# Performance work log

Measured on AMD Instinct MI355X. Metric: run time of the kernel, lower is better.

Reference implementation:

```python
import jax, jax.numpy as jnp
import numpy as np

NUM_HEADS = 16
ROPE_BASE = 2048.0


def _rope_tables(seq_len, head_dim, dtype):
    inv_freq = 1.0 / (ROPE_BASE ** (jnp.arange(0, head_dim, 2, dtype=jnp.float32) / head_dim))
    t = jnp.arange(seq_len, dtype=jnp.float32)
    freqs = jnp.einsum('i,j->ij', t, inv_freq)          # [N, D/2]
    emb = jnp.concatenate([freqs, freqs], axis=-1)       # [N, D]
    return jnp.cos(emb).astype(dtype), jnp.sin(emb).astype(dtype)


def _rotate_half(x):
    x1, x2 = jnp.split(x, 2, axis=-1)
    return jnp.concatenate([-x2, x1], axis=-1)


def setup_inputs() -> dict:
    key = jax.random.key(0)
    k1, k2, k3, k4 = jax.random.split(key, 4)
    B, N, C = 2, 2048, 1024
    x = jax.random.normal(k1, (B, N, C), dtype=jnp.float32)
    w_qkv = jax.random.normal(k2, (3 * C, C), dtype=jnp.float32) * (C ** -0.5)
    w_proj = jax.random.normal(k3, (C, C), dtype=jnp.float32) * (C ** -0.5)
    b_proj = jnp.zeros((C,), dtype=jnp.float32)
    key_padding_mask = jax.random.randint(k4, (B, N), 0, 2, dtype=jnp.int32)
    return {"x": x, "w_qkv": w_qkv, "w_proj": w_proj, "b_proj": b_proj,
            "key_padding_mask": key_padding_mask}


def reference(x, w_qkv, w_proj, b_proj, key_padding_mask):
    B, N, C = x.shape
    H = NUM_HEADS
    D = C // H
    scale = D ** -0.5

    qkv = x @ w_qkv.T                                    # [B, N, 3C]
    q, k, v = jnp.split(qkv, 3, axis=-1)
    # [B, N, C] -> [B, H, N, D]
    q = q.reshape(B, N, H, D).transpose(0, 2, 1, 3)
    k = k.reshape(B, N, H, D).transpose(0, 2, 1, 3)
    v = v.reshape(B, N, H, D).transpose(0, 2, 1, 3)

    cos, sin = _rope_tables(N, D, x.dtype)               # [N, D]
    q = q * cos + _rotate_half(q) * sin
    k = k * cos + _rotate_half(k) * sin

    attn = jnp.einsum('bhqd,bhkd->bhqk', q, k) * scale   # [B, H, N, N]
    mask = (key_padding_mask == 0)[:, None, None, :]     # [B, 1, 1, N]
    attn = jnp.where(mask, jnp.asarray(-1e9, attn.dtype), attn)
    attn = jax.nn.softmax(attn, axis=-1)

    out = jnp.einsum('bhqk,bhkd->bhqd', attn, v)         # [B, H, N, D]
    out = out.transpose(0, 2, 1, 3).reshape(B, N, C)
    return out @ w_proj.T + b_proj
```

## Files before the change

### kernel.cpp

```cpp
#include <hip/hip_runtime.h>


typedef __attribute__((ext_vector_type(8))) short          s16x8;
typedef __attribute__((ext_vector_type(8))) unsigned short u16x8;
typedef __attribute__((ext_vector_type(4))) unsigned short u16x4;
typedef __attribute__((ext_vector_type(4))) float          f32x4;

#define MFMA_BF16(a, b, c) __builtin_amdgcn_mfma_f32_16x16x32_bf16((a), (b), (c), 0, 0, 0)

#define GLD_TO_LDS(gp, lp) __builtin_amdgcn_global_load_lds(                  \
    (const __attribute__((address_space(1))) void*)(gp),                      \
    (__attribute__((address_space(3))) void*)(lp), 16, 0, 0)

__device__ __forceinline__ unsigned short f2bf(float f) {
    union { float f; unsigned int u; } v; v.f = f;
    unsigned int u = v.u;
    unsigned int r = u + 0x7FFFu + ((u >> 16) & 1u);
    return (unsigned short)(r >> 16);
}
__device__ __forceinline__ float bf2f(unsigned short h) {
    union { unsigned int u; float f; } v; v.u = ((unsigned int)h) << 16;
    return v.f;
}

__global__ __launch_bounds__(256) void prep(const float* __restrict__ x,
                                            const float* __restrict__ wqkv,
                                            const float* __restrict__ wproj,
                                            const int* __restrict__ m,
                                            unsigned short* __restrict__ xb,
                                            unsigned short* __restrict__ wqkvb,
                                            unsigned short* __restrict__ wprojb,
                                            float* __restrict__ fb) {
    int blk = blockIdx.x, tid = threadIdx.x;
    if (blk < 8192) {
        const float* src; unsigned short* dst; int i;
        if (blk < 4096)      { src = x;     dst = xb;     i = blk * 256 + tid; }
        else if (blk < 7168) { src = wqkv;  dst = wqkvb;  i = (blk - 4096) * 256 + tid; }
        else                 { src = wproj; dst = wprojb; i = (blk - 7168) * 256 + tid; }
        f32x4 v = ((const f32x4*)src)[i];
        u16x4 o;
        o[0] = f2bf(v[0]); o[1] = f2bf(v[1]); o[2] = f2bf(v[2]); o[3] = f2bf(v[3]);
        ((u16x4*)dst)[i] = o;
    } else {
        int i = (blk - 8192) * 256 + tid;
        fb[i] = (m[i] == 0) ? -1e5f : 0.0f;
    }
}

__global__ __launch_bounds__(256) void gemm_bt(const unsigned short* __restrict__ A,
                                               const unsigned short* __restrict__ B,
                                               unsigned short* __restrict__ C,
                                               int M, int N, int K) {
    __shared__ unsigned short Al[128][64];
    __shared__ unsigned short Bl[128][64];
    const int tid  = threadIdx.x;
    const int lane = tid & 63;
    const int qd   = lane >> 4;
    const int cc   = lane & 15;
    const int wave = tid >> 6;
    const int wr   = wave >> 1, wc = wave & 1;
    const int m0   = blockIdx.y * 128, n0 = blockIdx.x * 128;
    unsigned short* Alf = &Al[0][0];
    unsigned short* Blf = &Bl[0][0];

    f32x4 acc[4][4];
#pragma unroll
    for (int i = 0; i < 4; i++)
#pragma unroll
        for (int j = 0; j < 4; j++) acc[i][j] = (f32x4){0.f, 0.f, 0.f, 0.f};

    for (int k0 = 0; k0 < K; k0 += 64) {
#pragma unroll
        for (int t = 0; t < 4; t++) {
            int idx = t * 256 + tid;
            int row = idx >> 3, sg = (idx & 7) ^ (row & 7);
            GLD_TO_LDS(A + (size_t)(m0 + row) * K + k0 + sg * 8, Alf + idx * 8);
            GLD_TO_LDS(B + (size_t)(n0 + row) * K + k0 + sg * 8, Blf + idx * 8);
        }
        __syncthreads();
#pragma unroll
        for (int ks = 0; ks < 64; ks += 32) {
            const int s4 = ks >> 3;
            s16x8 af[4], bf[4];
#pragma unroll
            for (int i = 0; i < 4; i++) {
                int r = wr * 64 + i * 16 + cc;
                af[i] = *(const s16x8*)&Al[r][((s4 + qd) ^ (r & 7)) * 8];
            }
#pragma unroll
            for (int j = 0; j < 4; j++) {
                int r = wc * 64 + j * 16 + cc;
                bf[j] = *(const s16x8*)&Bl[r][((s4 + qd) ^ (r & 7)) * 8];
            }
#pragma unroll
            for (int i = 0; i < 4; i++)
#pragma unroll
                for (int j = 0; j < 4; j++)
                    acc[i][j] = MFMA_BF16(af[i], bf[j], acc[i][j]);
        }
        __syncthreads();
    }
#pragma unroll
    for (int i = 0; i < 4; i++)
#pragma unroll
        for (int j = 0; j < 4; j++)
#pragma unroll
            for (int r = 0; r < 4; r++) {
                int row = m0 + wr * 64 + i * 16 + qd * 4 + r;
                int col = n0 + wc * 64 + j * 16 + cc;
                C[(size_t)row * N + col] = f2bf(acc[i][j][r]);
            }
}

__global__ __launch_bounds__(256) void rope_scatter(const unsigned short* __restrict__ qkv,
                                                    unsigned short* __restrict__ Q,
                                                    unsigned short* __restrict__ Kg,
                                                    unsigned short* __restrict__ Vt) {
    const int N = 2048, H = 16, D = 64, C3 = 3072;
    __shared__ unsigned short vl[64][65];
    const int nt = blockIdx.x, h = blockIdx.y, b = blockIdx.z;
    const int n0 = nt * 64;
    const int tid = threadIdx.x;
    const size_t bh = (size_t)b * H + h;
#pragma unroll
    for (int it = 0; it < 2; it++) {
        int idx = tid + it * 256;
        int row = idx >> 3, seg = idx & 7;
        int d0 = seg * 8;
        int n = n0 + row;
        size_t rb = ((size_t)b * N + n) * C3;
        u16x8 qv = *(const u16x8*)&qkv[rb + h * 64 + d0];
        u16x8 qp = *(const u16x8*)&qkv[rb + h * 64 + (d0 ^ 32)];
        u16x8 kv = *(const u16x8*)&qkv[rb + 1024 + h * 64 + d0];
        u16x8 kp = *(const u16x8*)&qkv[rb + 1024 + h * 64 + (d0 ^ 32)];
        u16x8 vv = *(const u16x8*)&qkv[rb + 2048 + h * 64 + d0];
        u16x8 qo, ko;
        float sgn = (d0 < 32) ? -1.0f : 1.0f;
#pragma unroll
        for (int j = 0; j < 8; j++) {
            int jj = (d0 & 31) + j;
            float th = (float)n * exp2f(-0.34375f * (float)jj);
            float cth = cosf(th), sth = sinf(th);
            qo[j] = f2bf(bf2f(qv[j]) * cth + sgn * bf2f(qp[j]) * sth);
            ko[j] = f2bf(bf2f(kv[j]) * cth + sgn * bf2f(kp[j]) * sth);
            vl[row][d0 + j] = vv[j];
        }
        *(u16x8*)&Q[(bh * N + n) * D + d0]  = qo;
        *(u16x8*)&Kg[(bh * N + n) * D + d0] = ko;
    }
    __syncthreads();
#pragma unroll
    for (int it = 0; it < 2; it++) {
        int idx = tid + it * 256;
        int drow = idx >> 3, nseg = idx & 7;
        u16x8 ov;
#pragma unroll
        for (int j = 0; j < 8; j++) ov[j] = vl[nseg * 8 + j][drow];
        *(u16x8*)&Vt[(bh * D + drow) * N + n0 + nseg * 8] = ov;
    }
}

__global__ __launch_bounds__(256, 2) void flash_attn(const unsigned short* __restrict__ Q,
                                                     const unsigned short* __restrict__ Kg,
                                                     const unsigned short* __restrict__ Vt,
                                                     const float* __restrict__ fb,
                                                     unsigned short* __restrict__ Og) {
    const int N = 2048, H = 16, D = 64;
    const float SCL = 0.18033688f;
    __shared__ unsigned short Kl0[64][64], Kl1[64][64];
    __shared__ unsigned short Vl0[64][64], Vl1[64][64];
    __shared__ unsigned short Pl[4][32][76];
    const int tid  = threadIdx.x;
    const int lane = tid & 63;
    const int wave = tid >> 6;
    const int qd   = lane >> 4;
    const int cc   = lane & 15;
    const int qt = blockIdx.x, h = blockIdx.y, b = blockIdx.z;
    const int q0 = qt * 128;
    const size_t bh = (size_t)b * H + h;

    s16x8 qf[2][2];
#pragma unroll
    for (int fr = 0; fr < 2; fr++) {
        const unsigned short* Qb = Q + (bh * N + q0 + wave * 32 + fr * 16 + cc) * D;
        qf[fr][0] = *(const s16x8*)(Qb + qd * 8);
        qf[fr][1] = *(const s16x8*)(Qb + 32 + qd * 8);
    }

    s16x8 ones;
#pragma unroll
    for (int j = 0; j < 8; j++) ones[j] = (short)0x3F80;

    f32x4 o[2][4], lacc[2];
#pragma unroll
    for (int fr = 0; fr < 2; fr++) {
        lacc[fr] = (f32x4){0.f, 0.f, 0.f, 0.f};
#pragma unroll
        for (int db = 0; db < 4; db++) o[fr][db] = (f32x4){0.f, 0.f, 0.f, 0.f};
    }

    const unsigned short* Kbase = Kg + bh * N * D;
    const unsigned short* Vbase = Vt + bh * D * N;
    const float* fbase = fb + (size_t)b * N;
    const int row_s = tid >> 3, sg_s = (tid & 7) ^ ((tid >> 3) & 7);
    const int row_s2 = (tid + 256) >> 3, sg_s2 = (tid & 7) ^ (((tid + 256) >> 3) & 7);

    auto issue = [&](int k0, unsigned short* Kb, unsigned short* Vb) {
        GLD_TO_LDS(Kbase + (size_t)(k0 + row_s) * D + sg_s * 8,  Kb + tid * 8);
        GLD_TO_LDS(Vbase + (size_t)row_s * N + k0 + sg_s * 8,    Vb + tid * 8);
        GLD_TO_LDS(Kbase + (size_t)(k0 + row_s2) * D + sg_s2 * 8, Kb + (tid + 256) * 8);
        GLD_TO_LDS(Vbase + (size_t)row_s2 * N + k0 + sg_s2 * 8,   Vb + (tid + 256) * 8);
    };

    auto compute = [&](int k0, const unsigned short (*Kb)[64], const unsigned short (*Vb)[64]) {
        f32x4 fbv[4];
#pragma unroll
        for (int sub = 0; sub < 4; sub++)
            fbv[sub] = *(const f32x4*)(fbase + k0 + sub * 16 + qd * 4);

#pragma unroll
        for (int sub = 0; sub < 4; sub++) {
            int kr = sub * 16 + cc;
            s16x8 kf0 = *(const s16x8*)&Kb[kr][((0 + qd) ^ (kr & 7)) * 8];
            s16x8 kf1 = *(const s16x8*)&Kb[kr][((4 + qd) ^ (kr & 7)) * 8];
#pragma unroll
            for (int fr = 0; fr < 2; fr++) {
                f32x4 s = (f32x4){0.f, 0.f, 0.f, 0.f};
                s = MFMA_BF16(kf0, qf[fr][0], s);
                s = MFMA_BF16(kf1, qf[fr][1], s);
                float p0 = exp2f(fmaf(s[0], SCL, fbv[sub][0]));
                float p1 = exp2f(fmaf(s[1], SCL, fbv[sub][1]));
                float p2 = exp2f(fmaf(s[2], SCL, fbv[sub][2]));
                float p3 = exp2f(fmaf(s[3], SCL, fbv[sub][3]));
                unsigned int d0 = __builtin_amdgcn_perm(
                    __builtin_bit_cast(unsigned int, p1),
                    __builtin_bit_cast(unsigned int, p0), 0x07060302u);
                unsigned int d1 = __builtin_amdgcn_perm(
                    __builtin_bit_cast(unsigned int, p3),
                    __builtin_bit_cast(unsigned int, p2), 0x07060302u);
                unsigned long long w = ((unsigned long long)d1 << 32) | d0;
                *(unsigned long long*)&Pl[wave][fr * 16 + cc][sub * 16 + qd * 4] = w;
            }
        }

#pragma unroll
        for (int ks = 0; ks < 2; ks++) {
            s16x8 vfl[4];
#pragma unroll
            for (int db = 0; db < 4; db++) {
                int vr = db * 16 + cc;
                vfl[db] = *(const s16x8*)&Vb[vr][((ks * 4 + qd) ^ (vr & 7)) * 8];
            }
#pragma unroll
            for (int fr = 0; fr < 2; fr++) {
                s16x8 pf = *(const s16x8*)&Pl[wave][fr * 16 + cc][ks * 32 + qd * 8];
                lacc[fr] = MFMA_BF16(pf, ones, lacc[fr]);
#pragma unroll
                for (int db = 0; db < 4; db++)
                    o[fr][db] = MFMA_BF16(pf, vfl[db], o[fr][db]);
            }
        }
    };

    issue(0, &Kl0[0][0], &Vl0[0][0]);
    __syncthreads();
    for (int it = 0; it < 32; it += 2) {
        int k0 = it * 64;
        if (it + 1 < 32) issue(k0 + 64, &Kl1[0][0], &Vl1[0][0]);
        compute(k0, Kl0, Vl0);
        __syncthreads();
        if (it + 2 < 32) issue(k0 + 128, &Kl0[0][0], &Vl0[0][0]);
        compute(k0 + 64, Kl1, Vl1);
        __syncthreads();
    }

#pragma unroll
    for (int fr = 0; fr < 2; fr++) {
        float linv[4];
#pragma unroll
        for (int r = 0; r < 4; r++) linv[r] = 1.0f / lacc[fr][r];
#pragma unroll
        for (int db = 0; db < 4; db++)
#pragma unroll
            for (int r = 0; r < 4; r++) {
                int n = q0 + wave * 32 + fr * 16 + qd * 4 + r;
                Og[((size_t)b * N + n) * 1024 + h * 64 + db * 16 + cc] =
                    f2bf(o[fr][db][r] * linv[r]);
            }
    }
}

__global__ __launch_bounds__(256) void gemm_proj(const unsigned short* __restrict__ A,
                                                 const unsigned short* __restrict__ B,
                                                 float* __restrict__ C,
                                                 const float* __restrict__ bias) {
    const int NN = 1024, K = 1024;
    __shared__ unsigned short Al[128][64];
    __shared__ unsigned short Bl[64][64];
    const int tid  = threadIdx.x;
    const int lane = tid & 63;
    const int qd   = lane >> 4;
    const int cc   = lane & 15;
    const int wave = tid >> 6;
    const int wr   = wave >> 1, wc = wave & 1;
    const int m0   = blockIdx.y * 128, n0 = blockIdx.x * 64;
    unsigned short* Alf = &Al[0][0];
    unsigned short* Blf = &Bl[0][0];

    f32x4 acc[4][2];
#pragma unroll
    for (int i = 0; i < 4; i++)
#pragma unroll
        for (int j = 0; j < 2; j++) acc[i][j] = (f32x4){0.f, 0.f, 0.f, 0.f};

    for (int k0 = 0; k0 < K; k0 += 64) {
#pragma unroll
        for (int t = 0; t < 4; t++) {
            int idx = t * 256 + tid;
            int row = idx >> 3, sg = (idx & 7) ^ (row & 7);
            GLD_TO_LDS(A + (size_t)(m0 + row) * K + k0 + sg * 8, Alf + idx * 8);
        }
#pragma unroll
        for (int t = 0; t < 2; t++) {
            int idx = t * 256 + tid;
            int row = idx >> 3, sg = (idx & 7) ^ (row & 7);
            GLD_TO_LDS(B + (size_t)(n0 + row) * K + k0 + sg * 8, Blf + idx * 8);
        }
        __syncthreads();
#pragma unroll
        for (int ks = 0; ks < 64; ks += 32) {
            const int s4 = ks >> 3;
            s16x8 af[4], bf[2];
#pragma unroll
            for (int i = 0; i < 4; i++) {
                int r = wr * 64 + i * 16 + cc;
                af[i] = *(const s16x8*)&Al[r][((s4 + qd) ^ (r & 7)) * 8];
            }
#pragma unroll
            for (int j = 0; j < 2; j++) {
                int r = wc * 32 + j * 16 + cc;
                bf[j] = *(const s16x8*)&Bl[r][((s4 + qd) ^ (r & 7)) * 8];
            }
#pragma unroll
            for (int i = 0; i < 4; i++)
#pragma unroll
                for (int j = 0; j < 2; j++)
                    acc[i][j] = MFMA_BF16(af[i], bf[j], acc[i][j]);
        }
        __syncthreads();
    }
#pragma unroll
    for (int i = 0; i < 4; i++)
#pragma unroll
        for (int j = 0; j < 2; j++)
#pragma unroll
            for (int r = 0; r < 4; r++) {
                int row = m0 + wr * 64 + i * 16 + qd * 4 + r;
                int col = n0 + wc * 32 + j * 16 + cc;
                C[(size_t)row * NN + col] = acc[i][j][r] + bias[col];
            }
}

extern "C" void kernel_launch(void* const* d_in, const int* in_sizes, int n_in,
                              void* d_out, int out_size, void* d_ws, size_t ws_size,
                              hipStream_t stream) {
    const float* x      = (const float*)d_in[0];
    const float* w_qkv  = (const float*)d_in[1];
    const float* w_proj = (const float*)d_in[2];
    const float* b_proj = (const float*)d_in[3];
    const int*   mask   = (const int*)d_in[4];
    float* out = (float*)d_out;

    unsigned short* ws     = (unsigned short*)d_ws;
    unsigned short* xb     = ws;
    unsigned short* wqkvb  = xb     + (size_t)4096 * 1024;
    unsigned short* wprojb = wqkvb  + (size_t)3072 * 1024;
    unsigned short* qkv    = wprojb + (size_t)1024 * 1024;
    unsigned short* Qm     = qkv    + (size_t)4096 * 3072;
    unsigned short* Km     = Qm     + (size_t)32 * 2048 * 64;
    unsigned short* Vtm    = Km     + (size_t)32 * 2048 * 64;
    unsigned short* attno  = Vtm    + (size_t)32 * 2048 * 64;
    float*          fbias  = (float*)(attno + (size_t)4096 * 1024);

    prep<<<8208, 256, 0, stream>>>(x, w_qkv, w_proj, mask, xb, wqkvb, wprojb, fbias);
    gemm_bt<<<dim3(24, 32), 256, 0, stream>>>(xb, wqkvb, qkv, 4096, 3072, 1024);
    rope_scatter<<<dim3(32, 16, 2), 256, 0, stream>>>(qkv, Qm, Km, Vtm);
    flash_attn<<<dim3(16, 16, 2), 256, 0, stream>>>(Qm, Km, Vtm, fbias, attno);
    gemm_proj<<<dim3(16, 32), 256, 0, stream>>>(attno, wprojb, out, b_proj);
}
```

Measured before the change: 206.2 us.

## Fold mask into V and row-sum operand, prescale Q, interleave softmax with PV

```diff
diff --git a/kernel.cpp b/kernel.cpp
--- a/kernel.cpp
+++ b/kernel.cpp
@@ -30,7 +30,7 @@
                                             unsigned short* __restrict__ xb,
                                             unsigned short* __restrict__ wqkvb,
                                             unsigned short* __restrict__ wprojb,
-                                            float* __restrict__ fb) {
+                                            unsigned short* __restrict__ mb) {
     int blk = blockIdx.x, tid = threadIdx.x;
     if (blk < 8192) {
         const float* src; unsigned short* dst; int i;
@@ -43,7 +43,7 @@
         ((u16x4*)dst)[i] = o;
     } else {
         int i = (blk - 8192) * 256 + tid;
-        fb[i] = (m[i] == 0) ? -1e5f : 0.0f;
+        mb[i] = (m[i] == 0) ? (unsigned short)0 : (unsigned short)0x3F80;
     }
 }
 
@@ -113,10 +113,12 @@
 }
 
 __global__ __launch_bounds__(256) void rope_scatter(const unsigned short* __restrict__ qkv,
+                                                    const int* __restrict__ msk,
                                                     unsigned short* __restrict__ Q,
                                                     unsigned short* __restrict__ Kg,
                                                     unsigned short* __restrict__ Vt) {
     const int N = 2048, H = 16, D = 64, C3 = 3072;
+    const float SCL = 0.18033688f;
     __shared__ unsigned short vl[64][65];
     const int nt = blockIdx.x, h = blockIdx.y, b = blockIdx.z;
     const int n0 = nt * 64;
@@ -129,6 +131,7 @@
         int d0 = seg * 8;
         int n = n0 + row;
         size_t rb = ((size_t)b * N + n) * C3;
+        int keep = msk[(size_t)b * N + n];
         u16x8 qv = *(const u16x8*)&qkv[rb + h * 64 + d0];
         u16x8 qp = *(const u16x8*)&qkv[rb + h * 64 + (d0 ^ 32)];
         u16x8 kv = *(const u16x8*)&qkv[rb + 1024 + h * 64 + d0];
@@ -141,9 +144,9 @@
             int jj = (d0 & 31) + j;
             float th = (float)n * exp2f(-0.34375f * (float)jj);
             float cth = cosf(th), sth = sinf(th);
-            qo[j] = f2bf(bf2f(qv[j]) * cth + sgn * bf2f(qp[j]) * sth);
+            qo[j] = f2bf((bf2f(qv[j]) * cth + sgn * bf2f(qp[j]) * sth) * SCL);
             ko[j] = f2bf(bf2f(kv[j]) * cth + sgn * bf2f(kp[j]) * sth);
-            vl[row][d0 + j] = vv[j];
+            vl[row][d0 + j] = keep ? vv[j] : (unsigned short)0;
         }
         *(u16x8*)&Q[(bh * N + n) * D + d0]  = qo;
         *(u16x8*)&Kg[(bh * N + n) * D + d0] = ko;
@@ -163,10 +166,9 @@
 __global__ __launch_bounds__(256, 2) void flash_attn(const unsigned short* __restrict__ Q,
                                                      const unsigned short* __restrict__ Kg,
                                                      const unsigned short* __restrict__ Vt,
-                                                     const float* __restrict__ fb,
+                                                     const unsigned short* __restrict__ mb,
                                                      unsigned short* __restrict__ Og) {
     const int N = 2048, H = 16, D = 64;
-    const float SCL = 0.18033688f;
     __shared__ unsigned short Kl0[64][64], Kl1[64][64];
     __shared__ unsigned short Vl0[64][64], Vl1[64][64];
     __shared__ unsigned short Pl[4][32][76];
@@ -187,10 +189,6 @@
         qf[fr][1] = *(const s16x8*)(Qb + 32 + qd * 8);
     }
 
-    s16x8 ones;
-#pragma unroll
-    for (int j = 0; j < 8; j++) ones[j] = (short)0x3F80;
-
     f32x4 o[2][4], lacc[2];
 #pragma unroll
     for (int fr = 0; fr < 2; fr++) {
@@ -201,7 +199,7 @@
 
     const unsigned short* Kbase = Kg + bh * N * D;
     const unsigned short* Vbase = Vt + bh * D * N;
-    const float* fbase = fb + (size_t)b * N;
+    const unsigned short* mbase = mb + (size_t)b * N;
     const int row_s = tid >> 3, sg_s = (tid & 7) ^ ((tid >> 3) & 7);
     const int row_s2 = (tid + 256) >> 3, sg_s2 = (tid & 7) ^ (((tid + 256) >> 3) & 7);
 
@@ -213,11 +211,8 @@
     };
 
     auto compute = [&](int k0, const unsigned short (*Kb)[64], const unsigned short (*Vb)[64]) {
-        f32x4 fbv[4];
-#pragma unroll
-        for (int sub = 0; sub < 4; sub++)
-            fbv[sub] = *(const f32x4*)(fbase + k0 + sub * 16 + qd * 4);
-
+        f32x4 sst[4][2];
+        __builtin_amdgcn_s_setprio(1);
 #pragma unroll
         for (int sub = 0; sub < 4; sub++) {
             int kr = sub * 16 + cc;
@@ -227,39 +222,54 @@
             for (int fr = 0; fr < 2; fr++) {
                 f32x4 s = (f32x4){0.f, 0.f, 0.f, 0.f};
                 s = MFMA_BF16(kf0, qf[fr][0], s);
-                s = MFMA_BF16(kf1, qf[fr][1], s);
-                float p0 = exp2f(fmaf(s[0], SCL, fbv[sub][0]));
-                float p1 = exp2f(fmaf(s[1], SCL, fbv[sub][1]));
-                float p2 = exp2f(fmaf(s[2], SCL, fbv[sub][2]));
-                float p3 = exp2f(fmaf(s[3], SCL, fbv[sub][3]));
-                unsigned int d0 = __builtin_amdgcn_perm(
+                sst[sub][fr] = MFMA_BF16(kf1, qf[fr][1], s);
+            }
+        }
+        __builtin_amdgcn_s_setprio(0);
+
+        auto sm = [&](int sub) {
+#pragma unroll
+            for (int fr = 0; fr < 2; fr++) {
+                f32x4 s = sst[sub][fr];
+                float p0 = exp2f(s[0]);
+                float p1 = exp2f(s[1]);
+                float p2 = exp2f(s[2]);
+                float p3 = exp2f(s[3]);
+                unsigned int w0 = __builtin_amdgcn_perm(
                     __builtin_bit_cast(unsigned int, p1),
                     __builtin_bit_cast(unsigned int, p0), 0x07060302u);
-                unsigned int d1 = __builtin_amdgcn_perm(
+                unsigned int w1 = __builtin_amdgcn_perm(
                     __builtin_bit_cast(unsigned int, p3),
                     __builtin_bit_cast(unsigned int, p2), 0x07060302u);
-                unsigned long long w = ((unsigned long long)d1 << 32) | d0;
+                unsigned long long w = ((unsigned long long)w1 << 32) | w0;
                 *(unsigned long long*)&Pl[wave][fr * 16 + cc][sub * 16 + qd * 4] = w;
             }
-        }
-
-#pragma unroll
-        for (int ks = 0; ks < 2; ks++) {
+        };
+
+        auto pv = [&](int ks) {
+            s16x8 mf = *(const s16x8*)&mbase[k0 + ks * 32 + qd * 8];
             s16x8 vfl[4];
 #pragma unroll
             for (int db = 0; db < 4; db++) {
                 int vr = db * 16 + cc;
                 vfl[db] = *(const s16x8*)&Vb[vr][((ks * 4 + qd) ^ (vr & 7)) * 8];
             }
+            __builtin_amdgcn_s_setprio(1);
 #pragma unroll
             for (int fr = 0; fr < 2; fr++) {
                 s16x8 pf = *(const s16x8*)&Pl[wave][fr * 16 + cc][ks * 32 + qd * 8];
-                lacc[fr] = MFMA_BF16(pf, ones, lacc[fr]);
+                lacc[fr] = MFMA_BF16(pf, mf, lacc[fr]);
 #pragma unroll
                 for (int db = 0; db < 4; db++)
                     o[fr][db] = MFMA_BF16(pf, vfl[db], o[fr][db]);
             }
-        }
+            __builtin_amdgcn_s_setprio(0);
+        };
+
+        sm(0); sm(1);
+        pv(0);
+        sm(2); sm(3);
+        pv(1);
     };
 
     issue(0, &Kl0[0][0], &Vl0[0][0]);
@@ -380,11 +390,11 @@
     unsigned short* Km     = Qm     + (size_t)32 * 2048 * 64;
     unsigned short* Vtm    = Km     + (size_t)32 * 2048 * 64;
     unsigned short* attno  = Vtm    + (size_t)32 * 2048 * 64;
-    float*          fbias  = (float*)(attno + (size_t)4096 * 1024);
-
-    prep<<<8208, 256, 0, stream>>>(x, w_qkv, w_proj, mask, xb, wqkvb, wprojb, fbias);
+    unsigned short* maskbf = attno  + (size_t)4096 * 1024;
+
+    prep<<<8208, 256, 0, stream>>>(x, w_qkv, w_proj, mask, xb, wqkvb, wprojb, maskbf);
     gemm_bt<<<dim3(24, 32), 256, 0, stream>>>(xb, wqkvb, qkv, 4096, 3072, 1024);
-    rope_scatter<<<dim3(32, 16, 2), 256, 0, stream>>>(qkv, Qm, Km, Vtm);
-    flash_attn<<<dim3(16, 16, 2), 256, 0, stream>>>(Qm, Km, Vtm, fbias, attno);
+    rope_scatter<<<dim3(32, 16, 2), 256, 0, stream>>>(qkv, mask, Qm, Km, Vtm);
+    flash_attn<<<dim3(16, 16, 2), 256, 0, stream>>>(Qm, Km, Vtm, maskbf, attno);
     gemm_proj<<<dim3(16, 32), 256, 0, stream>>>(attno, wprojb, out, b_proj);
 }
```

Result: faster. 200.1 us (-3.0%).
